# Optimization experiments

Hardware: AMD Instinct MI355X
Metric: run time of the kernel (lower is better)

Reference implementation:

```python
import jax, jax.numpy as jnp
import numpy as np

B, S, H, NH = 8, 4096, 1024, 16
DH = H // NH  # head dim = 64
EPS = 1e-12


def setup_inputs() -> dict:
    key = jax.random.key(0)
    ks = jax.random.split(key, 10)
    sc = 1.0 / np.sqrt(H)
    return {
        "input_tensor": jax.random.normal(ks[0], (B, S, H), dtype=jnp.float32),
        "Wq": jax.random.normal(ks[1], (H, H), dtype=jnp.float32) * sc,
        "bq": jnp.zeros((H,), dtype=jnp.float32),
        "Wk": jax.random.normal(ks[2], (H, H), dtype=jnp.float32) * sc,
        "bk": jnp.zeros((H,), dtype=jnp.float32),
        "Wv": jax.random.normal(ks[3], (H, H), dtype=jnp.float32) * sc,
        "bv": jnp.zeros((H,), dtype=jnp.float32),
        "Wd": jax.random.normal(ks[4], (H, H), dtype=jnp.float32) * sc,
        "bd": jnp.zeros((H,), dtype=jnp.float32),
        "gamma": jnp.ones((H,), dtype=jnp.float32),
        "beta": jnp.zeros((H,), dtype=jnp.float32),
    }


def _heads(x):
    # [B,S,H] -> [B,NH,S,DH]
    return x.reshape(B, S, NH, DH).transpose(0, 2, 1, 3)


def reference(input_tensor, Wq, bq, Wk, bk, Wv, bv, Wd, bd, gamma, beta):
    q = _heads(input_tensor @ Wq + bq)  # [B,NH,S,DH]
    k = _heads(input_tensor @ Wk + bk)
    v = _heads(input_tensor @ Wv + bv)

    eq = jax.nn.elu(q)
    ek = jax.nn.elu(k)
    # L2-normalize per token along the head dim (matches norm over dim=3 of Q
    # and dim=2 of the [B,NH,DH,S]-permuted K in the torch code)
    qn = eq / jnp.linalg.norm(eq, axis=-1, keepdims=True)
    kn = ek / jnp.linalg.norm(ek, axis=-1, keepdims=True)

    kv = jnp.einsum("bhsd,bhse->bhde", kn, v)          # [B,NH,DH,DH]
    ctx = jnp.einsum("bhsd,bhde->bhse", qn, kv) / jnp.sqrt(jnp.float32(DH))
    ctx = ctx.transpose(0, 2, 1, 3).reshape(B, S, H)    # merge heads

    hidden = ctx @ Wd + bd
    x = hidden + input_tensor
    mu = jnp.mean(x, axis=-1, keepdims=True)
    var = jnp.mean(jnp.square(x - mu), axis=-1, keepdims=True)
    return (x - mu) / jnp.sqrt(var + EPS) * gamma + beta
```

## Files before the change

### kernel.cpp

```cpp
#include <hip/hip_runtime.h>
#include <cstdint>
#include <cstddef>

#define B_ 8
#define S_ 4096
#define H_ 1024
#define NH_ 16
#define DH_ 64
#define MTOK 32768

typedef unsigned short u16;
typedef __bf16 bf16x8 __attribute__((ext_vector_type(8)));
typedef u16 u16x8 __attribute__((ext_vector_type(8)));
typedef u16 u16x4 __attribute__((ext_vector_type(4)));
typedef float f32x4 __attribute__((ext_vector_type(4)));

#define DEVFN static __device__ __forceinline__

DEVFN float bf2f(u16 u) {
  union { uint32_t u; float f; } c; c.u = ((uint32_t)u) << 16; return c.f;
}
DEVFN u16 f2bf(float f) {
  union { float f; uint32_t u; } c; c.f = f;
  uint32_t r = c.u + 0x7fffu + ((c.u >> 16) & 1u);
  return (u16)(r >> 16);
}
DEVFN void gload16(const void* g, void* lds_p) {
  __builtin_amdgcn_global_load_lds(
      (const __attribute__((address_space(1))) void*)g,
      (__attribute__((address_space(3))) void*)lds_p, 16, 0, 0);
}

__global__ __launch_bounds__(256) void k_cvt_x(const float* __restrict__ x,
                                               u16* __restrict__ xb) {
  const size_t i = ((size_t)blockIdx.x * 256 + threadIdx.x) * 8;
  f32x4 a = *(const f32x4*)(x + i);
  f32x4 b = *(const f32x4*)(x + i + 4);
  u16x8 o;
#pragma unroll
  for (int j = 0; j < 4; ++j) { o[j] = f2bf(a[j]); o[4 + j] = f2bf(b[j]); }
  *(u16x8*)(xb + i) = o;
}

__global__ __launch_bounds__(256) void k_wt(const float* __restrict__ Wq,
                                            const float* __restrict__ Wk,
                                            const float* __restrict__ Wv,
                                            const float* __restrict__ Wd,
                                            u16* __restrict__ Wt,
                                            u16* __restrict__ Wdt) {
  const int n = blockIdx.x * 256 + threadIdx.x;
  const int kc = blockIdx.y;
  const int g = blockIdx.z;
  const float* W = (g == 0) ? Wq : (g == 1) ? Wk : (g == 2) ? Wv : Wd;
  u16x8 o;
#pragma unroll
  for (int j = 0; j < 8; ++j) o[j] = f2bf(W[(size_t)(kc * 8 + j) * 1024 + n]);
  u16* dst = (g < 3) ? (Wt + ((size_t)(g * 1024 + n)) * 1024 + kc * 8)
                     : (Wdt + (size_t)n * 1024 + kc * 8);
  *(u16x8*)dst = o;
}

template <int EPI>
__global__ __launch_bounds__(512, 2) void k_g(
    const u16* __restrict__ A, const u16* __restrict__ Bt,
    u16* __restrict__ o0, u16* __restrict__ o1, u16* __restrict__ o2,
    const float* __restrict__ b0, const float* __restrict__ b1,
    const float* __restrict__ b2) {
  __shared__ u16 As[2 * 128 * 32];
  __shared__ u16 Bs[2 * 256 * 32];
  const int tid = threadIdx.x;
  const int w = tid >> 6, l = tid & 63;
  const int wm = w >> 2, wn = w & 3;

  const int bid = (int)blockIdx.x;
  const int xcd = bid & 7, c = bid >> 3;
  int bx, by;
  if (EPI == 0) { by = c % 12; bx = xcd * 32 + c / 12; }
  else          { by = c & 3;  bx = xcd * 32 + (c >> 2); }

  const long row0 = (long)bx * 128;
  const long col0 = (long)by * 256;
  const u16* Bt2 = Bt + (EPI == 1 ? ((size_t)(row0 >> 12) << 20) : (size_t)0);

  f32x4 acc[4][4];
#pragma unroll
  for (int i = 0; i < 4; ++i)
#pragma unroll
    for (int j = 0; j < 4; ++j) acc[i][j] = (f32x4){0.f, 0.f, 0.f, 0.f};

  const int asl = ((tid & 3) ^ ((tid >> 3) & 3)) * 8;
  const u16* gA = A + (row0 + (tid >> 2)) * 1024 + asl;
  const u16* gB = Bt2 + (col0 + (tid >> 2)) * 1024 + asl;
  u16* lA = As + (w * 64) * 8;
  u16* lB = Bs + (w * 64) * 8;

  const int rsw = (((l >> 4) ^ ((l >> 1) & 3)) << 3);
  const int aoff = (wm * 64 + (l & 15)) * 32 + rsw;
  const int boff = (wn * 64 + (l & 15)) * 32 + rsw;

  for (int kt = 0; kt < 1024; kt += 64) {
    gload16(gA + kt, lA);
    gload16(gA + kt + 32, lA + 4096);
#pragma unroll
    for (int i = 0; i < 4; ++i) {
      const int go = (i & 1) * 131072 + (i >> 1) * 32 + kt;
      gload16(gB + go, lB + i * 4096);
    }
    __syncthreads();
#pragma unroll
    for (int kh = 0; kh < 2; ++kh) {
      bf16x8 af[4], bfr[4];
#pragma unroll
      for (int mi = 0; mi < 4; ++mi)
        af[mi] = *(const bf16x8*)(As + kh * 4096 + aoff + mi * 512);
#pragma unroll
      for (int ni = 0; ni < 4; ++ni)
        bfr[ni] = *(const bf16x8*)(Bs + kh * 8192 + boff + ni * 512);
#pragma unroll
      for (int mi = 0; mi < 4; ++mi)
#pragma unroll
        for (int ni = 0; ni < 4; ++ni)
          acc[mi][ni] = __builtin_amdgcn_mfma_f32_16x16x32_bf16(
              af[mi], bfr[ni], acc[mi][ni], 0, 0, 0);
    }
    __syncthreads();
  }

  const int rb = (int)row0 + wm * 64 + ((l >> 4) << 2);
  const int cb = (int)col0 + wn * 64 + (l & 15);
  if (EPI == 0) {
    const int seg = (int)(col0 >> 10);
    const int cl = cb & 1023;
    u16* outp = (seg == 0) ? o0 : (seg == 1) ? o1 : o2;
    const float* bias = (seg == 0) ? b0 : (seg == 1) ? b1 : b2;
#pragma unroll
    for (int mi = 0; mi < 4; ++mi)
#pragma unroll
      for (int ni = 0; ni < 4; ++ni) {
        const float bv_ = bias[cl + ni * 16];
#pragma unroll
        for (int r = 0; r < 4; ++r) {
          float v = acc[mi][ni][r] + bv_;
          if (seg < 2) v = v > 0.f ? v : expm1f(v);
          outp[(size_t)(rb + mi * 16 + r) * 1024 + cl + ni * 16] = f2bf(v);
        }
      }
  } else {
#pragma unroll
    for (int mi = 0; mi < 4; ++mi)
#pragma unroll
      for (int ni = 0; ni < 4; ++ni)
#pragma unroll
        for (int r = 0; r < 4; ++r)
          o0[(size_t)(rb + mi * 16 + r) * 1024 + cb + ni * 16] =
              f2bf(acc[mi][ni][r]);
  }
}

__global__ __launch_bounds__(256) void k_qn(u16* __restrict__ eq) {
  const int tid = threadIdx.x, w = tid >> 6, l = tid & 63;
  const long t = (long)blockIdx.x * 4 + w;
  const size_t base = (size_t)t * 1024 + (l >> 2) * 64 + (l & 3) * 16;
  u16x8 a = *(const u16x8*)(eq + base);
  u16x8 b = *(const u16x8*)(eq + base + 8);
  float f[16];
#pragma unroll
  for (int j = 0; j < 8; ++j) { f[j] = bf2f(a[j]); f[8 + j] = bf2f(b[j]); }
  float ss = 0.f;
#pragma unroll
  for (int j = 0; j < 16; ++j) ss += f[j] * f[j];
  ss += __shfl_xor(ss, 1);
  ss += __shfl_xor(ss, 2);
  const float rq = rsqrtf(ss);
  u16x8 oa, ob;
#pragma unroll
  for (int j = 0; j < 8; ++j) { oa[j] = f2bf(f[j] * rq); ob[j] = f2bf(f[8 + j] * rq); }
  *(u16x8*)(eq + base) = oa;
  *(u16x8*)(eq + base + 8) = ob;
}

__global__ __launch_bounds__(256) void k_kv(const u16* __restrict__ ek,
                                            const u16* __restrict__ vv,
                                            float* __restrict__ kvp) {
  __shared__ __align__(16) char lds[69632];
  const int tid = threadIdx.x, w = tid >> 6, l = tid & 63;
  const int bid = blockIdx.x;
  const int sc = bid & 3, h = (bid >> 2) & 15, b = bid >> 6;
  const int tp = l >> 3, dgrp = l & 7;
  char* myk = lds + w * 17408;
  char* myv = myk + 8192;
  const long Tw = (long)b * 4096 + sc * 1024 + w * 256;
  const int d0 = dgrp * 8;

  f32x4 acc[4][4];
#pragma unroll
  for (int i = 0; i < 4; ++i)
#pragma unroll
    for (int j = 0; j < 4; ++j) acc[i][j] = (f32x4){0.f, 0.f, 0.f, 0.f};

  for (int st = 0; st < 4; ++st) {
#pragma unroll
    for (int ro = 0; ro < 4; ++ro) {
      const int tl = ro * 16 + tp * 2;
      const long T = Tw + st * 64 + tl;
      const u16* kp = ek + (size_t)T * 1024 + h * 64 + d0;
      const u16* vp = vv + (size_t)T * 1024 + h * 64 + d0;
      u16x8 k0 = *(const u16x8*)kp, k1 = *(const u16x8*)(kp + 1024);
      u16x8 v0 = *(const u16x8*)vp, v1 = *(const u16x8*)(vp + 1024);
      float f0[8], f1[8], s0 = 0.f, s1 = 0.f;
#pragma unroll
      for (int j = 0; j < 8; ++j) {
        f0[j] = bf2f(k0[j]); s0 += f0[j] * f0[j];
        f1[j] = bf2f(k1[j]); s1 += f1[j] * f1[j];
      }
      s0 += __shfl_xor(s0, 1); s0 += __shfl_xor(s0, 2); s0 += __shfl_xor(s0, 4);
      s1 += __shfl_xor(s1, 1); s1 += __shfl_xor(s1, 2); s1 += __shfl_xor(s1, 4);
      const float r0 = rsqrtf(s0), r1 = rsqrtf(s1);
#pragma unroll
      for (int j = 0; j < 8; ++j) {
        const int d = d0 + j;
        const int sw = (d & 8) ? 32 : 0;
        *(uint32_t*)(myk + d * 128 + ((tl * 2) ^ sw)) =
            (uint32_t)f2bf(f0[j] * r0) | ((uint32_t)f2bf(f1[j] * r1) << 16);
        *(uint32_t*)(myv + d * 128 + ((tl * 2) ^ sw)) =
            (uint32_t)v0[j] | ((uint32_t)v1[j] << 16);
      }
    }
#pragma unroll
    for (int ksl = 0; ksl < 2; ++ksl) {
      const int sb = (ksl * 64 + (l >> 4) * 16) ^ ((l & 8) ? 32 : 0);
      bf16x8 a[4], bb[4];
#pragma unroll
      for (int mf = 0; mf < 4; ++mf)
        a[mf] = *(const bf16x8*)(myk + (mf * 16 + (l & 15)) * 128 + sb);
#pragma unroll
      for (int nf = 0; nf < 4; ++nf)
        bb[nf] = *(const bf16x8*)(myv + (nf * 16 + (l & 15)) * 128 + sb);
#pragma unroll
      for (int mf = 0; mf < 4; ++mf)
#pragma unroll
        for (int nf = 0; nf < 4; ++nf)
          acc[mf][nf] = __builtin_amdgcn_mfma_f32_16x16x32_bf16(
              a[mf], bb[nf], acc[mf][nf], 0, 0, 0);
    }
  }

  __syncthreads();
  float* lf = (float*)(lds + w * 17408);
#pragma unroll
  for (int mf = 0; mf < 4; ++mf)
#pragma unroll
    for (int nf = 0; nf < 4; ++nf)
#pragma unroll
      for (int r = 0; r < 4; ++r)
        lf[(mf * 16 + (l >> 4) * 4 + r) * 68 + nf * 16 + (l & 15)] =
            acc[mf][nf][r];
  __syncthreads();
  float* op = kvp + ((size_t)(sc * 8 + b) * 16 + h) * 4096;
  const float* l0 = (const float*)lds;
  const int dd = tid >> 2, eb = (tid & 3) * 16;
#pragma unroll
  for (int c = 0; c < 4; ++c) {
    f32x4 s = *(const f32x4*)(l0 + dd * 68 + eb + c * 4);
#pragma unroll
    for (int w2 = 1; w2 < 4; ++w2)
      s += *(const f32x4*)(l0 + w2 * 4352 + dd * 68 + eb + c * 4);
    *(f32x4*)(op + tid * 16 + c * 4) = s;
  }
}

__global__ __launch_bounds__(256) void k_m2(const float* __restrict__ kvp,
                                            const u16* __restrict__ Wdt,
                                            u16* __restrict__ M2t) {
  __shared__ __align__(16) u16 lds[12288];
  const int tid = threadIdx.x;
  const int w = tid >> 6, l = tid & 63;
  const int n0 = (int)blockIdx.x * 128, h = (int)blockIdx.y,
            b = (int)blockIdx.z;

#pragma unroll
  for (int g = 0; g < 4; ++g) {
    const int c = g * 256 + tid;
    gload16(Wdt + (size_t)(n0 + (c >> 3)) * 1024 + h * 64 + (c & 7) * 8,
            lds + 4096 + (g * 256 + w * 64) * 8);
  }
  const size_t kvbase = ((size_t)(b * 16 + h)) * 4096;
#pragma unroll
  for (int g = 0; g < 2; ++g) {
    const int c = g * 256 + tid;
    const float* p = kvp + kvbase + (size_t)(c >> 3) * 64 + (c & 7) * 8;
    f32x4 s0 = *(const f32x4*)p;
    f32x4 s1 = *(const f32x4*)(p + 4);
#pragma unroll
    for (int sc = 1; sc < 4; ++sc) {
      s0 += *(const f32x4*)(p + (size_t)sc * 524288);
      s1 += *(const f32x4*)(p + (size_t)sc * 524288 + 4);
    }
    u16x8 o;
#pragma unroll
    for (int j = 0; j < 4; ++j) { o[j] = f2bf(s0[j]); o[4 + j] = f2bf(s1[j]); }
    *(u16x8*)(lds + c * 8) = o;
  }
  __syncthreads();

  f32x4 acc[4][2];
#pragma unroll
  for (int i = 0; i < 4; ++i)
#pragma unroll
    for (int j = 0; j < 2; ++j) acc[i][j] = (f32x4){0.f, 0.f, 0.f, 0.f};

#pragma unroll
  for (int kh = 0; kh < 2; ++kh) {
    bf16x8 a[4], bb[2];
#pragma unroll
    for (int mf = 0; mf < 4; ++mf)
      a[mf] = *(const bf16x8*)(lds + (mf * 16 + (l & 15)) * 64 + kh * 32 +
                               (l >> 4) * 8);
#pragma unroll
    for (int nf = 0; nf < 2; ++nf)
      bb[nf] = *(const bf16x8*)(lds + 4096 +
                                (w * 32 + nf * 16 + (l & 15)) * 64 + kh * 32 +
                                (l >> 4) * 8);
#pragma unroll
    for (int mf = 0; mf < 4; ++mf)
#pragma unroll
      for (int nf = 0; nf < 2; ++nf)
        acc[mf][nf] = __builtin_amdgcn_mfma_f32_16x16x32_bf16(
            a[mf], bb[nf], acc[mf][nf], 0, 0, 0);
  }

  u16* outb = M2t + ((size_t)b << 20) + h * 64;
#pragma unroll
  for (int mf = 0; mf < 4; ++mf)
#pragma unroll
    for (int nf = 0; nf < 2; ++nf) {
      const int col = w * 32 + nf * 16 + (l & 15);
      u16x4 o;
#pragma unroll
      for (int r = 0; r < 4; ++r) o[r] = f2bf(acc[mf][nf][r] * 0.125f);
      *(u16x4*)(outb + (size_t)(n0 + col) * 1024 + mf * 16 + (l >> 4) * 4) = o;
    }
}

__global__ __launch_bounds__(256) void k_ln(const u16* __restrict__ hid,
                                            const u16* __restrict__ xb,
                                            const float* __restrict__ bd,
                                            const float* __restrict__ g,
                                            const float* __restrict__ be,
                                            float* __restrict__ out) {
  const int tid = threadIdx.x, w = tid >> 6, l = tid & 63;
  const size_t base = (size_t)blockIdx.x * 1024 + tid * 4;
  u16x4 h4 = *(const u16x4*)(hid + base);
  u16x4 x4 = *(const u16x4*)(xb + base);
  f32x4 bd4 = *(const f32x4*)(bd + tid * 4);
  float v[4];
#pragma unroll
  for (int j = 0; j < 4; ++j) v[j] = bf2f(h4[j]) + bf2f(x4[j]) + bd4[j];
  float s = v[0] + v[1] + v[2] + v[3];
  float ss = v[0] * v[0] + v[1] * v[1] + v[2] * v[2] + v[3] * v[3];
#pragma unroll
  for (int o = 32; o > 0; o >>= 1) {
    s += __shfl_xor(s, o);
    ss += __shfl_xor(ss, o);
  }
  __shared__ float red[8];
  if (l == 0) { red[w] = s; red[w + 4] = ss; }
  __syncthreads();
  s = red[0] + red[1] + red[2] + red[3];
  ss = red[4] + red[5] + red[6] + red[7];
  const float mu = s * (1.0f / 1024.0f);
  const float var = ss * (1.0f / 1024.0f) - mu * mu;
  const float rstd = rsqrtf(var + 1e-12f);
  f32x4 g4 = *(const f32x4*)(g + tid * 4);
  f32x4 b4 = *(const f32x4*)(be + tid * 4);
  f32x4 o;
#pragma unroll
  for (int j = 0; j < 4; ++j) o[j] = (v[j] - mu) * rstd * g4[j] + b4[j];
  *(f32x4*)(out + base) = o;
}

extern "C" void kernel_launch(void* const* d_in, const int* in_sizes, int n_in,
                              void* d_out, int out_size, void* d_ws,
                              size_t ws_size, hipStream_t stream) {
  const float* X = (const float*)d_in[0];
  const float* Wq = (const float*)d_in[1];
  const float* bq = (const float*)d_in[2];
  const float* Wk = (const float*)d_in[3];
  const float* bk = (const float*)d_in[4];
  const float* Wv = (const float*)d_in[5];
  const float* bv = (const float*)d_in[6];
  const float* Wd = (const float*)d_in[7];
  const float* bd = (const float*)d_in[8];
  const float* gamma = (const float*)d_in[9];
  const float* beta = (const float*)d_in[10];
  float* out = (float*)d_out;

  char* ws = (char*)d_ws;
  u16* Xb = (u16*)(ws);
  u16* Wt = (u16*)(ws + 67108864);
  u16* eq = (u16*)(ws + 73400320);
  u16* ek = (u16*)(ws + 140509184);
  u16* vb = (u16*)(ws + 207618048);
  u16* Wdt = (u16*)(ws + 274726912);
  float* kvp = (float*)(ws + 276824064);
  u16* M2t = (u16*)(ws + 285212672);

  k_cvt_x<<<16384, 256, 0, stream>>>(X, Xb);
  k_wt<<<dim3(4, 128, 4), 256, 0, stream>>>(Wq, Wk, Wv, Wd, Wt, Wdt);
  k_g<0><<<3072, 512, 0, stream>>>(Xb, Wt, eq, ek, vb, bq, bk, bv);
  k_qn<<<8192, 256, 0, stream>>>(eq);
  k_kv<<<512, 256, 0, stream>>>(ek, vb, kvp);
  k_m2<<<dim3(8, 16, 8), 256, 0, stream>>>(kvp, Wdt, M2t);
  k_g<1><<<1024, 512, 0, stream>>>(eq, M2t, ek, nullptr, nullptr, nullptr,
                                   nullptr, nullptr);
  k_ln<<<32768, 256, 0, stream>>>(ek, Xb, bd, gamma, beta, out);
}
```

Baseline: 492.4 us.

## Double-buffer LDS tiles in GEMM kernel to overlap global loads with MFMA

Splits the shared-memory A/B tiles into two buffers and issues the next k-tile's global-to-LDS loads before computing on the current tile. Each iteration now needs one explicit vmcnt wait and one raw barrier instead of two __syncthreads. This is meant to hide global load latency behind MFMA work. LDS use doubles to 96 KB per block, which may limit residency at the requested 2 blocks per CU.

```diff
diff --git a/kernel.cpp b/kernel.cpp
--- a/kernel.cpp
+++ b/kernel.cpp
@@ -30,6 +30,10 @@
       (const __attribute__((address_space(1))) void*)g,
       (__attribute__((address_space(3))) void*)lds_p, 16, 0, 0);
 }
+
+#define FENCE asm volatile("" ::: "memory")
+#define RAWBAR do { FENCE; __builtin_amdgcn_s_barrier(); FENCE; } while (0)
+#define WAITVM0 asm volatile("s_waitcnt vmcnt(0)" ::: "memory")
 
 __global__ __launch_bounds__(256) void k_cvt_x(const float* __restrict__ x,
                                                u16* __restrict__ xb) {
@@ -66,8 +70,8 @@
     u16* __restrict__ o0, u16* __restrict__ o1, u16* __restrict__ o2,
     const float* __restrict__ b0, const float* __restrict__ b1,
     const float* __restrict__ b2) {
-  __shared__ u16 As[2 * 128 * 32];
-  __shared__ u16 Bs[2 * 256 * 32];
+  __shared__ u16 As[2][2 * 128 * 32];
+  __shared__ u16 Bs[2][2 * 256 * 32];
   const int tid = threadIdx.x;
   const int w = tid >> 6, l = tid & 63;
   const int wm = w >> 2, wn = w & 3;
@@ -91,31 +95,38 @@
   const int asl = ((tid & 3) ^ ((tid >> 3) & 3)) * 8;
   const u16* gA = A + (row0 + (tid >> 2)) * 1024 + asl;
   const u16* gB = Bt2 + (col0 + (tid >> 2)) * 1024 + asl;
-  u16* lA = As + (w * 64) * 8;
-  u16* lB = Bs + (w * 64) * 8;
+  const int ldst = (w * 64) * 8;
+
+#define STAGE(buf, kt)                                                   \
+  do {                                                                   \
+    gload16(gA + (kt), &As[buf][ldst]);                                  \
+    gload16(gA + (kt) + 32, &As[buf][4096 + ldst]);                      \
+    _Pragma("unroll") for (int i = 0; i < 4; ++i) {                      \
+      const int go = (i & 1) * 131072 + (i >> 1) * 32 + (kt);            \
+      gload16(gB + go, &Bs[buf][i * 4096 + ldst]);                       \
+    }                                                                    \
+  } while (0)
 
   const int rsw = (((l >> 4) ^ ((l >> 1) & 3)) << 3);
   const int aoff = (wm * 64 + (l & 15)) * 32 + rsw;
   const int boff = (wn * 64 + (l & 15)) * 32 + rsw;
 
-  for (int kt = 0; kt < 1024; kt += 64) {
-    gload16(gA + kt, lA);
-    gload16(gA + kt + 32, lA + 4096);
-#pragma unroll
-    for (int i = 0; i < 4; ++i) {
-      const int go = (i & 1) * 131072 + (i >> 1) * 32 + kt;
-      gload16(gB + go, lB + i * 4096);
-    }
-    __syncthreads();
+  STAGE(0, 0);
+  WAITVM0;
+  RAWBAR;
+
+  for (int t = 0; t < 16; ++t) {
+    const int buf = t & 1;
+    if (t + 1 < 16) STAGE(buf ^ 1, (t + 1) * 64);
 #pragma unroll
     for (int kh = 0; kh < 2; ++kh) {
       bf16x8 af[4], bfr[4];
 #pragma unroll
       for (int mi = 0; mi < 4; ++mi)
-        af[mi] = *(const bf16x8*)(As + kh * 4096 + aoff + mi * 512);
+        af[mi] = *(const bf16x8*)(&As[buf][kh * 4096 + aoff + mi * 512]);
 #pragma unroll
       for (int ni = 0; ni < 4; ++ni)
-        bfr[ni] = *(const bf16x8*)(Bs + kh * 8192 + boff + ni * 512);
+        bfr[ni] = *(const bf16x8*)(&Bs[buf][kh * 8192 + boff + ni * 512]);
 #pragma unroll
       for (int mi = 0; mi < 4; ++mi)
 #pragma unroll
@@ -123,8 +134,12 @@
           acc[mi][ni] = __builtin_amdgcn_mfma_f32_16x16x32_bf16(
               af[mi], bfr[ni], acc[mi][ni], 0, 0, 0);
     }
-    __syncthreads();
-  }
+    if (t + 1 < 16) {
+      WAITVM0;
+      RAWBAR;
+    }
+  }
+#undef STAGE
 
   const int rb = (int)row0 + wm * 64 + ((l >> 4) << 2);
   const int cb = (int)col0 + wn * 64 + (l & 15);
```

Result: slower. 616.5 us (+25.2%).
